# Kernel tuning notes

Hardware: AMD Instinct MI355X
Metric: run time of the kernel (lower is better)

## Reference

```python
import jax, jax.numpy as jnp
import numpy as np

D_MODEL, D_LOW, NUM_BINS = 512, 64, 39
DIST_MIN, DIST_MAX = 2.0, 22.0
BIN_WIDTH = (DIST_MAX - DIST_MIN) / (NUM_BINS - 1)
LN_EPS = 1e-5


def setup_inputs() -> dict:
    key = jax.random.key(0)
    ks = jax.random.split(key, 10)
    B, N = 2, 768
    h_res = jax.random.normal(ks[0], (B, N, D_MODEL), dtype=jnp.float32)
    # scale coords so pairwise distances span the [2, 22] bin range
    x_true = jax.random.normal(ks[1], (B, N, 3), dtype=jnp.float32) * 5.0
    token_pad_mask = jnp.ones((B, N), dtype=jnp.float32)
    s = 1.0 / np.sqrt(D_MODEL)
    return {
        "h_res": h_res,
        "x_true": x_true,
        "token_pad_mask": token_pad_mask,
        "ln_w": jnp.ones((D_MODEL,), jnp.float32),
        "ln_b": jnp.zeros((D_MODEL,), jnp.float32),
        "wu_w": jax.random.normal(ks[2], (D_LOW, D_MODEL), jnp.float32) * s,
        "wu_b": jnp.zeros((D_LOW,), jnp.float32),
        "wv_w": jax.random.normal(ks[3], (D_LOW, D_MODEL), jnp.float32) * s,
        "wv_b": jnp.zeros((D_LOW,), jnp.float32),
        "wb_w": jax.random.normal(ks[4], (NUM_BINS, D_LOW), jnp.float32) * (1.0 / np.sqrt(D_LOW)),
        "wb_b": jnp.zeros((NUM_BINS,), jnp.float32),
    }


def _layernorm(x, w, b):
    mu = jnp.mean(x, axis=-1, keepdims=True)
    var = jnp.mean(jnp.square(x - mu), axis=-1, keepdims=True)
    return (x - mu) * jax.lax.rsqrt(var + LN_EPS) * w + b


def reference(h_res, x_true, token_pad_mask, ln_w, ln_b, wu_w, wu_b, wv_w, wv_b, wb_w, wb_b):
    B, N, _ = h_res.shape
    # pairwise distances -> target bins (trunc-to-int then clamp, as torch .long())
    diff = x_true[:, :, None, :] - x_true[:, None, :, :]          # [B,N,N,3]
    d_true = jnp.sqrt(jnp.sum(diff * diff, axis=-1))               # [B,N,N]
    target = jnp.clip(((d_true - DIST_MIN) / BIN_WIDTH).astype(jnp.int32), 0, NUM_BINS - 1)

    h = _layernorm(h_res, ln_w, ln_b)
    U = h @ wu_w.T + wu_b                                          # [B,N,d_low]
    V = h @ wv_w.T + wv_b                                          # [B,N,d_low]
    # logits[b,i,j,k] = sum_c U[b,i,c] V[b,j,c] Wb[k,c] + bb[k]
    logits = jnp.einsum("bic,bjc,kc->bijk", U, V, wb_w) + wb_b     # [B,N,N,K]
    logp = jax.nn.log_softmax(logits, axis=-1)
    ce = -jnp.take_along_axis(logp, target[..., None], axis=-1)[..., 0]  # [B,N,N]

    mask = (token_pad_mask[:, :, None] * token_pad_mask[:, None, :]) > 0  # [B,N,N] bool
    counts = jnp.sum(mask, axis=(1, 2))                            # [B]
    per_sample = jnp.sum(jnp.where(mask, ce, 0.0), axis=(1, 2)) / jnp.maximum(counts, 1)
    valid = counts > 0
    total_count = jnp.sum(valid)
    loss = jnp.sum(jnp.where(valid, per_sample, 0.0)) / jnp.maximum(total_count, 1)
    return loss
```

## Files before the change

kernel.cpp:

```cpp
#include <hip/hip_runtime.h>
#include <hip/hip_bf16.h>
#include <math.h>

#define D_MODEL 512
#define D_LOW   64
#define NBINS   39
#define LOG2E   1.4426950408889634f
#define LN2     0.6931471805599453f
#define IT      2

typedef __attribute__((ext_vector_type(8))) short short8;
typedef __attribute__((ext_vector_type(4))) float floatx4;

__global__ __launch_bounds__(256) void prep_kernel(
    const float* __restrict__ ln_w, const float* __restrict__ ln_b,
    const float* __restrict__ wu_w, const float* __restrict__ wu_b,
    const float* __restrict__ wv_w, const float* __restrict__ wv_b,
    __hip_bfloat16* __restrict__ w2bf, float* __restrict__ w2sum,
    float* __restrict__ b2) {
  __shared__ float red[8];
  const int tid = threadIdx.x;
  const int o = blockIdx.x;
  const bool isU = (o < 64);
  const float* wrow = isU ? (wu_w + o * D_MODEL) : (wv_w + (o - 64) * D_MODEL);
  const float scale = isU ? LOG2E : 1.0f;

  float s1 = 0.f, s2 = 0.f;
  #pragma unroll
  for (int cc = 0; cc < 2; ++cc) {
    const int c = tid + cc * 256;
    const float w  = wrow[c];
    const float w2 = w * ln_w[c] * scale;
    const __hip_bfloat16 hb = __float2bfloat16(w2);
    w2bf[o * D_MODEL + c] = hb;
    s1 += __bfloat162float(hb);
    s2 += w * ln_b[c];
  }
  #pragma unroll
  for (int off = 32; off; off >>= 1) {
    s1 += __shfl_xor(s1, off);
    s2 += __shfl_xor(s2, off);
  }
  const int wave = tid >> 6, lane = tid & 63;
  if (lane == 0) { red[wave] = s1; red[4 + wave] = s2; }
  __syncthreads();
  if (tid == 0) {
    w2sum[o] = red[0] + red[1] + red[2] + red[3];
    const float ss2 = red[4] + red[5] + red[6] + red[7];
    b2[o] = scale * ((isU ? wu_b[o] : wv_b[o - 64]) + ss2);
  }
}

__global__ __launch_bounds__(64) void lnproj_kernel(
    const float* __restrict__ h_res, const __hip_bfloat16* __restrict__ w2bf,
    const float* __restrict__ w2sum, const float* __restrict__ b2,
    float* __restrict__ U, __hip_bfloat16* __restrict__ Vbf, int N) {
  const int lane = threadIdx.x;
  const int q = lane >> 4, ln16 = lane & 15;
  const int rt = blockIdx.x >> 3, og = blockIdx.x & 7;
  const int row0 = rt * 16;
  const float* hp = h_res + (size_t)(row0 + ln16) * D_MODEL + q * 8;

  short8 abf[16];
  float sum = 0.f, ssq = 0.f;
  #pragma unroll
  for (int kc = 0; kc < 16; ++kc) {
    const floatx4 x0 = *reinterpret_cast<const floatx4*>(hp + kc * 32);
    const floatx4 x1 = *reinterpret_cast<const floatx4*>(hp + kc * 32 + 4);
    short8 a;
    #pragma unroll
    for (int e = 0; e < 4; ++e) {
      sum += x0[e]; ssq += x0[e] * x0[e];
      const __hip_bfloat16 hb = __float2bfloat16(x0[e]);
      a[e] = *reinterpret_cast<const short*>(&hb);
    }
    #pragma unroll
    for (int e = 0; e < 4; ++e) {
      sum += x1[e]; ssq += x1[e] * x1[e];
      const __hip_bfloat16 hb = __float2bfloat16(x1[e]);
      a[4 + e] = *reinterpret_cast<const short*>(&hb);
    }
    abf[kc] = a;
  }
  sum += __shfl_xor(sum, 16); sum += __shfl_xor(sum, 32);
  ssq += __shfl_xor(ssq, 16); ssq += __shfl_xor(ssq, 32);
  const float mu  = sum * (1.0f / (float)D_MODEL);
  const float var = ssq * (1.0f / (float)D_MODEL) - mu * mu;
  const float rs  = rsqrtf(var + 1e-5f);
  float mu_r[4], rs_r[4];
  #pragma unroll
  for (int r = 0; r < 4; ++r) {
    mu_r[r] = __shfl(mu, q * 4 + r);
    rs_r[r] = __shfl(rs, q * 4 + r);
  }

  const int out = og * 16 + ln16;
  const short* wp = reinterpret_cast<const short*>(w2bf);
  floatx4 acc = (floatx4){0.f, 0.f, 0.f, 0.f};
  #pragma unroll
  for (int kc = 0; kc < 16; ++kc) {
    const short8 bfr = *reinterpret_cast<const short8*>(
        wp + (size_t)out * D_MODEL + kc * 32 + q * 8);
    acc = __builtin_amdgcn_mfma_f32_16x16x32_bf16(abf[kc], bfr, acc, 0, 0, 0);
  }

  const float ws = w2sum[out];
  const float bb = b2[out];
  #pragma unroll
  for (int r = 0; r < 4; ++r) {
    const int rowg = row0 + q * 4 + r;
    const float val = rs_r[r] * acc[r] - mu_r[r] * rs_r[r] * ws + bb;
    if (out < 64) {
      U[(size_t)rowg * D_LOW + out] = val;
    } else {
      Vbf[(size_t)rowg * D_LOW + (out - 64)] = __float2bfloat16(val);
    }
  }
}

__global__ __launch_bounds__(256) void pair_fused_kernel(
    const float* __restrict__ U, const __hip_bfloat16* __restrict__ Vbf,
    const float* __restrict__ wb_w, const float* __restrict__ wb_b,
    const float* __restrict__ x_true, const float* __restrict__ pmask,
    float* __restrict__ part, int N) {
  __shared__ float rbuf[8];
  const int b    = blockIdx.y >> 1;
  const int half = blockIdx.y & 1;
  const int i0   = blockIdx.x * IT;
  const int tid  = threadIdx.x;
  const int wave = tid >> 6, lane = tid & 63;
  const int q = lane >> 4, ln16 = lane & 15;
  const int jbase = half * 384 + wave * 96;
  const int q4 = q * 4;

  float xj0[6], xj1[6], xj2[6], pmj[6];
  #pragma unroll
  for (int sl = 0; sl < 6; ++sl) {
    const int jr = jbase + (sl >> 1) * 32 + (sl & 1) * 16 + ln16;
    const int rowj = b * N + jr;
    xj0[sl] = x_true[rowj * 3 + 0];
    xj1[sl] = x_true[rowj * 3 + 1];
    xj2[sl] = x_true[rowj * 3 + 2];
    pmj[sl] = pmask[rowj];
  }
  const float BW = (22.0f - 2.0f) / 38.0f;
  int tbv[IT][6];
  #pragma unroll
  for (int it = 0; it < IT; ++it) {
    const int rowi = b * N + i0 + it;
    const float xi0 = x_true[rowi * 3 + 0];
    const float xi1 = x_true[rowi * 3 + 1];
    const float xi2 = x_true[rowi * 3 + 2];
    const float pmi = pmask[rowi];
    #pragma unroll
    for (int sl = 0; sl < 6; ++sl) {
      const float dx = xi0 - xj0[sl];
      const float dy = xi1 - xj1[sl];
      const float dz = xi2 - xj2[sl];
      const float d  = sqrtf(dx * dx + dy * dy + dz * dz);
      int tb = (int)((d - 2.0f) / BW);
      tb = tb < 0 ? 0 : (tb > NBINS - 1 ? NBINS - 1 : tb);
      tbv[it][sl] = (pmi * pmj[sl] > 0.f) ? tb : -1;
    }
  }

  floatx4 u[IT][4];
  #pragma unroll
  for (int it = 0; it < IT; ++it) {
    const float* Up = U + (size_t)(b * N + i0 + it) * D_LOW;
    #pragma unroll
    for (int s = 0; s < 2; ++s) {
      u[it][s * 2 + 0] = *reinterpret_cast<const floatx4*>(Up + s * 32 + q * 8);
      u[it][s * 2 + 1] = *reinterpret_cast<const floatx4*>(Up + s * 32 + q * 8 + 4);
    }
  }
  short8 wfrag[IT][3][2];
  #pragma unroll
  for (int t = 0; t < 3; ++t) {
    const int n = t * 16 + ln16;
    const bool valid = (n < NBINS);
    const float* wrow = wb_w + (size_t)(valid ? n : 0) * D_LOW;
    #pragma unroll
    for (int s = 0; s < 2; ++s) {
      const floatx4 w0 = *reinterpret_cast<const floatx4*>(wrow + s * 32 + q * 8);
      const floatx4 w1 = *reinterpret_cast<const floatx4*>(wrow + s * 32 + q * 8 + 4);
      #pragma unroll
      for (int it = 0; it < IT; ++it) {
        short8 f;
        #pragma unroll
        for (int e = 0; e < 4; ++e) {
          const float v0 = valid ? u[it][s * 2 + 0][e] * w0[e] : 0.f;
          const float v1 = valid ? u[it][s * 2 + 1][e] * w1[e] : 0.f;
          const __hip_bfloat16 h0 = __float2bfloat16(v0);
          const __hip_bfloat16 h1 = __float2bfloat16(v1);
          f[e]     = *reinterpret_cast<const short*>(&h0);
          f[4 + e] = *reinterpret_cast<const short*>(&h1);
        }
        wfrag[it][t][s] = f;
      }
    }
  }

  floatx4 bias_init[3];
  #pragma unroll
  for (int t = 0; t < 3; ++t)
    #pragma unroll
    for (int r = 0; r < 4; ++r) {
      const int bin = t * 16 + q * 4 + r;
      bias_init[t][r] = (bin < NBINS) ? LOG2E * wb_b[bin] : -INFINITY;
    }

  const short* Vp = reinterpret_cast<const short*>(Vbf) + (size_t)b * N * D_LOW;
  float ce_sum = 0.f, cnt_sum = 0.f;

  short8 v[2][2];
  #pragma unroll
  for (int tt = 0; tt < 2; ++tt) {
    const size_t jr = jbase + tt * 16 + ln16;
    v[tt][0] = *reinterpret_cast<const short8*>(Vp + jr * D_LOW + q * 8);
    v[tt][1] = *reinterpret_cast<const short8*>(Vp + jr * D_LOW + 32 + q * 8);
  }

  #pragma unroll
  for (int g = 0; g < 3; ++g) {
    short8 vn[2][2];
    if (g < 2) {
      const int jb = jbase + (g + 1) * 32;
      #pragma unroll
      for (int tt = 0; tt < 2; ++tt) {
        const size_t jr = jb + tt * 16 + ln16;
        vn[tt][0] = *reinterpret_cast<const short8*>(Vp + jr * D_LOW + q * 8);
        vn[tt][1] = *reinterpret_cast<const short8*>(Vp + jr * D_LOW + 32 + q * 8);
      }
    }

    #pragma unroll
    for (int it = 0; it < IT; ++it) {
      floatx4 f[2][3];
      #pragma unroll
      for (int tt = 0; tt < 2; ++tt)
        #pragma unroll
        for (int t = 0; t < 3; ++t) {
          floatx4 a = bias_init[t];
          a = __builtin_amdgcn_mfma_f32_16x16x32_bf16(wfrag[it][t][0], v[tt][0], a, 0, 0, 0);
          a = __builtin_amdgcn_mfma_f32_16x16x32_bf16(wfrag[it][t][1], v[tt][1], a, 0, 0, 0);
          f[tt][t] = a;
        }

      #pragma unroll
      for (int tt = 0; tt < 2; ++tt) {
        const int tb  = tbv[it][g * 2 + tt];
        const int tbq = tb - q4;
        float s0 = 0.f, s1 = 0.f, s2 = 0.f, s3 = 0.f, lt = 0.f;
        #pragma unroll
        for (int t = 0; t < 3; ++t) {
          const floatx4 fv = f[tt][t];
          s0 += __builtin_amdgcn_exp2f(fv[0]);
          s1 += __builtin_amdgcn_exp2f(fv[1]);
          s2 += __builtin_amdgcn_exp2f(fv[2]);
          s3 += __builtin_amdgcn_exp2f(fv[3]);
          lt += (tbq == t * 16 + 0) ? fv[0] : 0.f;
          lt += (tbq == t * 16 + 1) ? fv[1] : 0.f;
          lt += (tbq == t * 16 + 2) ? fv[2] : 0.f;
          lt += (tbq == t * 16 + 3) ? fv[3] : 0.f;
        }
        float ssum = (s0 + s1) + (s2 + s3);
        ssum += __shfl_xor(ssum, 16); ssum += __shfl_xor(ssum, 32);
        const float ok = (tb >= 0) ? 1.f : 0.f;
        ce_sum  += ok * LN2 * (__builtin_amdgcn_logf(ssum) - 4.0f * lt);
        cnt_sum += ok;
      }
    }

    if (g < 2) {
      #pragma unroll
      for (int tt = 0; tt < 2; ++tt) {
        v[tt][0] = vn[tt][0]; v[tt][1] = vn[tt][1];
      }
    }
  }

  #pragma unroll
  for (int off = 32; off; off >>= 1) {
    ce_sum  += __shfl_xor(ce_sum, off);
    cnt_sum += __shfl_xor(cnt_sum, off);
  }
  if (lane == 0) { rbuf[wave] = ce_sum; rbuf[4 + wave] = cnt_sum; }
  __syncthreads();
  if (tid == 0) {
    const size_t slot = ((size_t)blockIdx.y * gridDim.x + blockIdx.x) * 2;
    part[slot + 0] = rbuf[0] + rbuf[1] + rbuf[2] + rbuf[3];
    part[slot + 1] = rbuf[4] + rbuf[5] + rbuf[6] + rbuf[7];
  }
}

__global__ __launch_bounds__(256) void finalize_kernel(
    const float* __restrict__ part, float* __restrict__ out, int NP, int B) {
  __shared__ float red[8];
  const int tid = threadIdx.x, wave = tid >> 6, lane = tid & 63;
  float loss = 0.f, vcount = 0.f;
  for (int b = 0; b < B; ++b) {
    float ce = 0.f, cnt = 0.f;
    for (int e = tid; e < 2 * NP; e += 256) {
      const size_t base = ((size_t)b * 2 * NP + e) * 2;
      ce  += part[base + 0];
      cnt += part[base + 1];
    }
    #pragma unroll
    for (int off = 32; off; off >>= 1) {
      ce  += __shfl_xor(ce, off);
      cnt += __shfl_xor(cnt, off);
    }
    if (lane == 0) { red[wave] = ce; red[4 + wave] = cnt; }
    __syncthreads();
    if (tid == 0) {
      const float s = red[0] + red[1] + red[2] + red[3];
      const float c = red[4] + red[5] + red[6] + red[7];
      if (c > 0.f) { loss += s / fmaxf(c, 1.f); vcount += 1.f; }
    }
    __syncthreads();
  }
  if (tid == 0) out[0] = (vcount > 0.f) ? loss / vcount : 0.f;
}

extern "C" void kernel_launch(void* const* d_in, const int* in_sizes, int n_in,
                              void* d_out, int out_size, void* d_ws, size_t ws_size,
                              hipStream_t stream) {
  const float* h_res  = (const float*)d_in[0];
  const float* x_true = (const float*)d_in[1];
  const float* pmask  = (const float*)d_in[2];
  const float* ln_w   = (const float*)d_in[3];
  const float* ln_b   = (const float*)d_in[4];
  const float* wu_w   = (const float*)d_in[5];
  const float* wu_b   = (const float*)d_in[6];
  const float* wv_w   = (const float*)d_in[7];
  const float* wv_b   = (const float*)d_in[8];
  const float* wb_w   = (const float*)d_in[9];
  const float* wb_b   = (const float*)d_in[10];

  const int B  = 2;
  const int N  = in_sizes[2] / B;
  const int BN = B * N;
  const int NP = N / IT;

  float* U = (float*)d_ws;
  __hip_bfloat16* Vbf = (__hip_bfloat16*)(U + (size_t)BN * D_LOW);
  float* part = (float*)(Vbf + (size_t)BN * D_LOW);
  __hip_bfloat16* w2bf = (__hip_bfloat16*)(part + (size_t)2 * B * NP * 2);
  float* w2sum = (float*)(w2bf + 128 * D_MODEL);
  float* b2    = w2sum + 128;

  prep_kernel<<<128, 256, 0, stream>>>(ln_w, ln_b, wu_w, wu_b, wv_w, wv_b,
                                       w2bf, w2sum, b2);
  lnproj_kernel<<<(BN / 16) * 8, 64, 0, stream>>>(h_res, w2bf, w2sum, b2,
                                                  U, Vbf, N);
  pair_fused_kernel<<<dim3(NP, 2 * B), 256, 0, stream>>>(
      U, Vbf, wb_w, wb_b, x_true, pmask, part, N);
  finalize_kernel<<<1, 256, 0, stream>>>(part, (float*)d_out, NP, B);
}
```

Before: 119.9 us.

## Retile pair kernel to four i-rows per block and fuse finalize via last-block atomic

Each block now handles four i rows and a quarter of the j range, with each wave covering 48 j columns. All V fragments are loaded once and reused across the four i rows, and the software prefetch loop is removed. The separate finalize launch is replaced by an atomic counter, reset in prep_kernel, so the last finishing block performs the final reduction. This cuts one kernel launch and increases V reuse per MFMA. In exchange it holds more wfrag registers per thread, which may lower occupancy, and adds an atomic plus threadfence at the end of every block.

```diff
diff --git a/kernel.cpp b/kernel.cpp
--- a/kernel.cpp
+++ b/kernel.cpp
@@ -7,7 +7,7 @@
 #define NBINS   39
 #define LOG2E   1.4426950408889634f
 #define LN2     0.6931471805599453f
-#define IT      2
+#define IT      4
 
 typedef __attribute__((ext_vector_type(8))) short short8;
 typedef __attribute__((ext_vector_type(4))) float floatx4;
@@ -17,10 +17,11 @@
     const float* __restrict__ wu_w, const float* __restrict__ wu_b,
     const float* __restrict__ wv_w, const float* __restrict__ wv_b,
     __hip_bfloat16* __restrict__ w2bf, float* __restrict__ w2sum,
-    float* __restrict__ b2) {
+    float* __restrict__ b2, int* __restrict__ ctr) {
   __shared__ float red[8];
   const int tid = threadIdx.x;
   const int o = blockIdx.x;
+  if (o == 0 && tid == 0) *ctr = 0;
   const bool isU = (o < 64);
   const float* wrow = isU ? (wu_w + o * D_MODEL) : (wv_w + (o - 64) * D_MODEL);
   const float scale = isU ? LOG2E : 1.0f;
@@ -122,29 +123,30 @@
     const float* __restrict__ U, const __hip_bfloat16* __restrict__ Vbf,
     const float* __restrict__ wb_w, const float* __restrict__ wb_b,
     const float* __restrict__ x_true, const float* __restrict__ pmask,
-    float* __restrict__ part, int N) {
+    float* __restrict__ part, int* __restrict__ ctr,
+    float* __restrict__ out, int N) {
   __shared__ float rbuf[8];
-  const int b    = blockIdx.y >> 1;
-  const int half = blockIdx.y & 1;
+  __shared__ int is_last;
+  const int b    = blockIdx.y >> 2;
+  const int qtr  = blockIdx.y & 3;
   const int i0   = blockIdx.x * IT;
   const int tid  = threadIdx.x;
   const int wave = tid >> 6, lane = tid & 63;
   const int q = lane >> 4, ln16 = lane & 15;
-  const int jbase = half * 384 + wave * 96;
+  const int jbase = qtr * 192 + wave * 48;
   const int q4 = q * 4;
 
-  float xj0[6], xj1[6], xj2[6], pmj[6];
-  #pragma unroll
-  for (int sl = 0; sl < 6; ++sl) {
-    const int jr = jbase + (sl >> 1) * 32 + (sl & 1) * 16 + ln16;
-    const int rowj = b * N + jr;
-    xj0[sl] = x_true[rowj * 3 + 0];
-    xj1[sl] = x_true[rowj * 3 + 1];
-    xj2[sl] = x_true[rowj * 3 + 2];
-    pmj[sl] = pmask[rowj];
+  float xj0[3], xj1[3], xj2[3], pmj[3];
+  #pragma unroll
+  for (int tl = 0; tl < 3; ++tl) {
+    const int rowj = b * N + jbase + tl * 16 + ln16;
+    xj0[tl] = x_true[rowj * 3 + 0];
+    xj1[tl] = x_true[rowj * 3 + 1];
+    xj2[tl] = x_true[rowj * 3 + 2];
+    pmj[tl] = pmask[rowj];
   }
   const float BW = (22.0f - 2.0f) / 38.0f;
-  int tbv[IT][6];
+  int tbv[IT][3];
   #pragma unroll
   for (int it = 0; it < IT; ++it) {
     const int rowi = b * N + i0 + it;
@@ -153,14 +155,14 @@
     const float xi2 = x_true[rowi * 3 + 2];
     const float pmi = pmask[rowi];
     #pragma unroll
-    for (int sl = 0; sl < 6; ++sl) {
-      const float dx = xi0 - xj0[sl];
-      const float dy = xi1 - xj1[sl];
-      const float dz = xi2 - xj2[sl];
+    for (int tl = 0; tl < 3; ++tl) {
+      const float dx = xi0 - xj0[tl];
+      const float dy = xi1 - xj1[tl];
+      const float dz = xi2 - xj2[tl];
       const float d  = sqrtf(dx * dx + dy * dy + dz * dz);
       int tb = (int)((d - 2.0f) / BW);
       tb = tb < 0 ? 0 : (tb > NBINS - 1 ? NBINS - 1 : tb);
-      tbv[it][sl] = (pmi * pmj[sl] > 0.f) ? tb : -1;
+      tbv[it][tl] = (pmi * pmj[tl] > 0.f) ? tb : -1;
     }
   }
 
@@ -211,72 +213,48 @@
     }
 
   const short* Vp = reinterpret_cast<const short*>(Vbf) + (size_t)b * N * D_LOW;
+  short8 v[3][2];
+  #pragma unroll
+  for (int tl = 0; tl < 3; ++tl) {
+    const size_t jr = jbase + tl * 16 + ln16;
+    v[tl][0] = *reinterpret_cast<const short8*>(Vp + jr * D_LOW + q * 8);
+    v[tl][1] = *reinterpret_cast<const short8*>(Vp + jr * D_LOW + 32 + q * 8);
+  }
+
   float ce_sum = 0.f, cnt_sum = 0.f;
-
-  short8 v[2][2];
-  #pragma unroll
-  for (int tt = 0; tt < 2; ++tt) {
-    const size_t jr = jbase + tt * 16 + ln16;
-    v[tt][0] = *reinterpret_cast<const short8*>(Vp + jr * D_LOW + q * 8);
-    v[tt][1] = *reinterpret_cast<const short8*>(Vp + jr * D_LOW + 32 + q * 8);
-  }
-
-  #pragma unroll
-  for (int g = 0; g < 3; ++g) {
-    short8 vn[2][2];
-    if (g < 2) {
-      const int jb = jbase + (g + 1) * 32;
+  #pragma unroll
+  for (int tl = 0; tl < 3; ++tl) {
+    #pragma unroll
+    for (int it = 0; it < IT; ++it) {
+      floatx4 f[3];
       #pragma unroll
-      for (int tt = 0; tt < 2; ++tt) {
-        const size_t jr = jb + tt * 16 + ln16;
-        vn[tt][0] = *reinterpret_cast<const short8*>(Vp + jr * D_LOW + q * 8);
-        vn[tt][1] = *reinterpret_cast<const short8*>(Vp + jr * D_LOW + 32 + q * 8);
-      }
-    }
-
-    #pragma unroll
-    for (int it = 0; it < IT; ++it) {
-      floatx4 f[2][3];
+      for (int t = 0; t < 3; ++t) {
+        floatx4 a = bias_init[t];
+        a = __builtin_amdgcn_mfma_f32_16x16x32_bf16(wfrag[it][t][0], v[tl][0], a, 0, 0, 0);
+        a = __builtin_amdgcn_mfma_f32_16x16x32_bf16(wfrag[it][t][1], v[tl][1], a, 0, 0, 0);
+        f[t] = a;
+      }
+
+      const int tb  = tbv[it][tl];
+      const int tbq = tb - q4;
+      float s0 = 0.f, s1 = 0.f, s2 = 0.f, s3 = 0.f, lt = 0.f;
       #pragma unroll
-      for (int tt = 0; tt < 2; ++tt)
-        #pragma unroll
-        for (int t = 0; t < 3; ++t) {
-          floatx4 a = bias_init[t];
-          a = __builtin_amdgcn_mfma_f32_16x16x32_bf16(wfrag[it][t][0], v[tt][0], a, 0, 0, 0);
-          a = __builtin_amdgcn_mfma_f32_16x16x32_bf16(wfrag[it][t][1], v[tt][1], a, 0, 0, 0);
-          f[tt][t] = a;
-        }
-
-      #pragma unroll
-      for (int tt = 0; tt < 2; ++tt) {
-        const int tb  = tbv[it][g * 2 + tt];
-        const int tbq = tb - q4;
-        float s0 = 0.f, s1 = 0.f, s2 = 0.f, s3 = 0.f, lt = 0.f;
-        #pragma unroll
-        for (int t = 0; t < 3; ++t) {
-          const floatx4 fv = f[tt][t];
-          s0 += __builtin_amdgcn_exp2f(fv[0]);
-          s1 += __builtin_amdgcn_exp2f(fv[1]);
-          s2 += __builtin_amdgcn_exp2f(fv[2]);
-          s3 += __builtin_amdgcn_exp2f(fv[3]);
-          lt += (tbq == t * 16 + 0) ? fv[0] : 0.f;
-          lt += (tbq == t * 16 + 1) ? fv[1] : 0.f;
-          lt += (tbq == t * 16 + 2) ? fv[2] : 0.f;
-          lt += (tbq == t * 16 + 3) ? fv[3] : 0.f;
-        }
-        float ssum = (s0 + s1) + (s2 + s3);
-        ssum += __shfl_xor(ssum, 16); ssum += __shfl_xor(ssum, 32);
-        const float ok = (tb >= 0) ? 1.f : 0.f;
-        ce_sum  += ok * LN2 * (__builtin_amdgcn_logf(ssum) - 4.0f * lt);
-        cnt_sum += ok;
-      }
-    }
-
-    if (g < 2) {
-      #pragma unroll
-      for (int tt = 0; tt < 2; ++tt) {
-        v[tt][0] = vn[tt][0]; v[tt][1] = vn[tt][1];
-      }
+      for (int t = 0; t < 3; ++t) {
+        const floatx4 fv = f[t];
+        s0 += __builtin_amdgcn_exp2f(fv[0]);
+        s1 += __builtin_amdgcn_exp2f(fv[1]);
+        s2 += __builtin_amdgcn_exp2f(fv[2]);
+        s3 += __builtin_amdgcn_exp2f(fv[3]);
+        lt += (tbq == t * 16 + 0) ? fv[0] : 0.f;
+        lt += (tbq == t * 16 + 1) ? fv[1] : 0.f;
+        lt += (tbq == t * 16 + 2) ? fv[2] : 0.f;
+        lt += (tbq == t * 16 + 3) ? fv[3] : 0.f;
+      }
+      float ssum = (s0 + s1) + (s2 + s3);
+      ssum += __shfl_xor(ssum, 16); ssum += __shfl_xor(ssum, 32);
+      const float ok = (tb >= 0) ? 1.f : 0.f;
+      ce_sum  += ok * LN2 * (__builtin_amdgcn_logf(ssum) - 4.0f * lt);
+      cnt_sum += ok;
     }
   }
 
@@ -287,40 +265,47 @@
   }
   if (lane == 0) { rbuf[wave] = ce_sum; rbuf[4 + wave] = cnt_sum; }
   __syncthreads();
+
+  const int NP = gridDim.x;
+  const int nblocks = NP * gridDim.y;
   if (tid == 0) {
-    const size_t slot = ((size_t)blockIdx.y * gridDim.x + blockIdx.x) * 2;
+    const size_t slot = ((size_t)blockIdx.y * NP + blockIdx.x) * 2;
     part[slot + 0] = rbuf[0] + rbuf[1] + rbuf[2] + rbuf[3];
     part[slot + 1] = rbuf[4] + rbuf[5] + rbuf[6] + rbuf[7];
-  }
-}
-
-__global__ __launch_bounds__(256) void finalize_kernel(
-    const float* __restrict__ part, float* __restrict__ out, int NP, int B) {
-  __shared__ float red[8];
-  const int tid = threadIdx.x, wave = tid >> 6, lane = tid & 63;
-  float loss = 0.f, vcount = 0.f;
-  for (int b = 0; b < B; ++b) {
-    float ce = 0.f, cnt = 0.f;
-    for (int e = tid; e < 2 * NP; e += 256) {
-      const size_t base = ((size_t)b * 2 * NP + e) * 2;
-      ce  += part[base + 0];
-      cnt += part[base + 1];
-    }
-    #pragma unroll
-    for (int off = 32; off; off >>= 1) {
-      ce  += __shfl_xor(ce, off);
-      cnt += __shfl_xor(cnt, off);
-    }
-    if (lane == 0) { red[wave] = ce; red[4 + wave] = cnt; }
-    __syncthreads();
-    if (tid == 0) {
-      const float s = red[0] + red[1] + red[2] + red[3];
-      const float c = red[4] + red[5] + red[6] + red[7];
-      if (c > 0.f) { loss += s / fmaxf(c, 1.f); vcount += 1.f; }
-    }
-    __syncthreads();
-  }
-  if (tid == 0) out[0] = (vcount > 0.f) ? loss / vcount : 0.f;
+    __threadfence();
+    const int t = atomicAdd(ctr, 1);
+    is_last = (t == nblocks - 1) ? 1 : 0;
+  }
+  __syncthreads();
+
+  if (is_last) {
+    __threadfence();
+    __shared__ float red[8];
+    float loss = 0.f, vcount = 0.f;
+    const int nper = 4 * NP;
+    for (int bb = 0; bb < 2; ++bb) {
+      float ce = 0.f, cnt = 0.f;
+      for (int e = tid; e < nper; e += 256) {
+        const size_t base = ((size_t)bb * nper + e) * 2;
+        ce  += part[base + 0];
+        cnt += part[base + 1];
+      }
+      #pragma unroll
+      for (int off = 32; off; off >>= 1) {
+        ce  += __shfl_xor(ce, off);
+        cnt += __shfl_xor(cnt, off);
+      }
+      if (lane == 0) { red[wave] = ce; red[4 + wave] = cnt; }
+      __syncthreads();
+      if (tid == 0) {
+        const float s = red[0] + red[1] + red[2] + red[3];
+        const float c = red[4] + red[5] + red[6] + red[7];
+        if (c > 0.f) { loss += s / fmaxf(c, 1.f); vcount += 1.f; }
+      }
+      __syncthreads();
+    }
+    if (tid == 0) out[0] = (vcount > 0.f) ? loss / vcount : 0.f;
+  }
 }
 
 extern "C" void kernel_launch(void* const* d_in, const int* in_sizes, int n_in,
@@ -346,15 +331,15 @@
   float* U = (float*)d_ws;
   __hip_bfloat16* Vbf = (__hip_bfloat16*)(U + (size_t)BN * D_LOW);
   float* part = (float*)(Vbf + (size_t)BN * D_LOW);
-  __hip_bfloat16* w2bf = (__hip_bfloat16*)(part + (size_t)2 * B * NP * 2);
+  int* ctr = (int*)(part + (size_t)4 * B * NP * 2);
+  __hip_bfloat16* w2bf = (__hip_bfloat16*)(ctr + 64);
   float* w2sum = (float*)(w2bf + 128 * D_MODEL);
   float* b2    = w2sum + 128;
 
   prep_kernel<<<128, 256, 0, stream>>>(ln_w, ln_b, wu_w, wu_b, wv_w, wv_b,
-                                       w2bf, w2sum, b2);
+                                       w2bf, w2sum, b2, ctr);
   lnproj_kernel<<<(BN / 16) * 8, 64, 0, stream>>>(h_res, w2bf, w2sum, b2,
                                                   U, Vbf, N);
-  pair_fused_kernel<<<dim3(NP, 2 * B), 256, 0, stream>>>(
-      U, Vbf, wb_w, wb_b, x_true, pmask, part, N);
-  finalize_kernel<<<1, 256, 0, stream>>>(part, (float*)d_out, NP, B);
+  pair_fused_kernel<<<dim3(NP, 4 * B), 256, 0, stream>>>(
+      U, Vbf, wb_w, wb_b, x_true, pmask, part, ctr, (float*)d_out, N);
 }
```

Result: slower. 155.3 us (+29.6%).
